# Optimization experiments

Hardware: AMD Instinct MI355X
Metric: run time of the kernel (lower is better)

## Reference

```python
import jax, jax.numpy as jnp
import numpy as np

B, S, H, D = 4, 2048, 16, 64
E = H * D  # embed_dim = 1024


def setup_inputs() -> dict:
    key = jax.random.key(0)
    kq, kk, kv, kw, kb = jax.random.split(key, 5)
    query = jax.random.normal(kq, (B, S, H, D), dtype=jnp.float32)
    key_t = jax.random.normal(kk, (B, S, H, D), dtype=jnp.float32)
    value = jax.random.normal(kv, (B, S, H, D), dtype=jnp.float32)
    qkv_proj = jnp.zeros((1,), dtype=jnp.float32)  # unused arg in original forward
    # causal mask (0 = masked), matching masked_fill(attn_mask == 0, -inf)
    attn_mask = jnp.tril(jnp.ones((S, S), dtype=jnp.int32))
    bound = 1.0 / np.sqrt(E)
    out_w = jax.random.uniform(kw, (E, E), jnp.float32, -bound, bound)
    out_b = jax.random.uniform(kb, (E,), jnp.float32, -bound, bound)
    return {"query": query, "key": key_t, "value": value, "qkv_proj": qkv_proj,
            "attn_mask": attn_mask, "out_w": out_w, "out_b": out_b}


def reference(query, key, value, qkv_proj, attn_mask, out_w, out_b):
    # flatten heads: module does single-head attention over embed_dim
    q = query.reshape(B, S, E) * (float(E) ** -0.5)  # scaling uses embed_dim, per source
    k = key.reshape(B, S, E)
    v = value.reshape(B, S, E)
    scores = jnp.einsum('bqe,bke->bqk', q, k)  # [B,S,S]
    scores = jnp.where(attn_mask[None, :, :] == 0, -jnp.inf, scores)
    # safe softmax: subtract max, exp, normalize
    probs = jax.nn.softmax(scores, axis=-1)
    attn_out = jnp.einsum('bqk,bke->bqe', probs, v)  # [B,S,E]
    return attn_out @ out_w.T + out_b
```

## Files before the change

### kernel.cpp

```cpp
#include <hip/hip_runtime.h>


typedef __attribute__((ext_vector_type(8))) short bf16x8;
typedef __attribute__((ext_vector_type(4))) float floatx4;

#define MFMA16(a, b, c) __builtin_amdgcn_mfma_f32_16x16x32_bf16((a), (b), (c), 0, 0, 0)

#define B_ 4
#define S_ 2048
#define E_ 1024

static __device__ __forceinline__ unsigned short f2bf(float f) {
  unsigned int u = __float_as_uint(f);
  u += 0x7FFFu + ((u >> 16) & 1u);
  return (unsigned short)(u >> 16);
}
static __device__ __forceinline__ float bf2f(unsigned short h) {
  return __uint_as_float(((unsigned int)h) << 16);
}

#define STAGE_TILE_64(dst, srcbase, LD, k0, w, l)                              \
  _Pragma("unroll")                                                            \
  for (int i_ = 0; i_ < 4; ++i_) {                                             \
    int c_ = i_ * 256 + (w) * 64 + (l);                                        \
    int row_ = c_ >> 3, cg_ = c_ & 7;                                          \
    int col_ = (cg_ ^ (row_ & 7)) * 8;                                         \
    __builtin_amdgcn_global_load_lds(                                          \
        (const __attribute__((address_space(1))) unsigned int*)((srcbase) +    \
            (size_t)row_ * (LD) + (k0) + col_),                                \
        (__attribute__((address_space(3))) unsigned int*)((dst) +              \
            (size_t)(i_ * 256 + (w) * 64) * 8),                                \
        16, 0, 0);                                                             \
  }

static __device__ __forceinline__ const bf16x8* frag_at(
    const unsigned short* base, int row, int cg) {
  return (const bf16x8*)(base + (size_t)row * 64 + ((cg ^ (row & 7)) * 8));
}

__global__ void cvt_all_kernel(const float* __restrict__ Q,
                               const float* __restrict__ K,
                               const float* __restrict__ W,
                               unsigned short* __restrict__ Qbf,
                               unsigned short* __restrict__ Kbf,
                               unsigned short* __restrict__ Wbf) {
  const int nQK = (B_ * S_ * E_) / 4;
  const int nW  = (E_ * E_) / 4;
  const int total = 2 * nQK + nW;
  int i = blockIdx.x * blockDim.x + threadIdx.x;
  int stride = gridDim.x * blockDim.x;
  for (; i < total; i += stride) {
    const float* src; unsigned short* dst; float sc; int j;
    if (i < nQK)            { src = Q; dst = Qbf; sc = 0.03125f; j = i; }
    else if (i < 2 * nQK)   { src = K; dst = Kbf; sc = 1.0f; j = i - nQK; }
    else                    { src = W; dst = Wbf; sc = 1.0f; j = i - 2 * nQK; }
    float4 v = ((const float4*)src)[j];
    ushort4 o;
    o.x = f2bf(v.x * sc); o.y = f2bf(v.y * sc);
    o.z = f2bf(v.z * sc); o.w = f2bf(v.w * sc);
    ((ushort4*)dst)[j] = o;
  }
}

__global__ void transpose_v_kernel(const float* __restrict__ V,
                                   unsigned short* __restrict__ Vt) {
  __shared__ float tile[32][33];
  int bid = blockIdx.x;
  int eb = (bid & 31) * 32;
  int sb = ((bid >> 5) & 63) * 32;
  int b  = bid >> 11;
  int tx = threadIdx.x & 31, ty = threadIdx.x >> 5;
  const float* src = V + ((size_t)(b * S_ + sb)) * E_ + eb;
#pragma unroll
  for (int i = 0; i < 4; ++i) {
    int sl = ty + i * 8;
    tile[sl][tx] = src[(size_t)sl * E_ + tx];
  }
  __syncthreads();
  unsigned short* dst = Vt + ((size_t)(b * E_ + eb)) * S_ + sb;
#pragma unroll
  for (int i = 0; i < 4; ++i) {
    int el = ty + i * 8;
    dst[(size_t)el * S_ + tx] = f2bf(tile[tx][el]);
  }
}

__global__ __launch_bounds__(256, 4) void qk_kernel(
    const unsigned short* __restrict__ A,
    const unsigned short* __restrict__ Bw,
    unsigned short* __restrict__ SP,
    float* __restrict__ rsp) {
  __shared__ unsigned short At[128 * 64];
  __shared__ unsigned short Bt[128 * 64];
  __shared__ float rs_l[2][128];
  const int bid0 = blockIdx.x;
  const int bid = (bid0 & 7) * 68 + (bid0 >> 3);
  const int b = bid / 136;
  const int ti = bid - b * 136;
  float fr = sqrtf(8.0f * (float)ti + 1.0f);
  int trow = (int)((fr - 1.0f) * 0.5f);
  if ((trow + 1) * (trow + 2) / 2 <= ti) ++trow;
  else if (trow * (trow + 1) / 2 > ti) --trow;
  const int tcol = ti - trow * (trow + 1) / 2;
  const int bm = trow * 128, bn = tcol * 128;

  const int tid = threadIdx.x;
  const int w = tid >> 6, l = tid & 63;
  const int l15 = l & 15, l4 = l >> 4;
  const int wr = w >> 1, wc = w & 1;
  const unsigned short* Ab = A + (size_t)b * S_ * E_ + (size_t)bm * E_;
  const unsigned short* Bb = Bw + (size_t)b * S_ * E_ + (size_t)bn * E_;

  floatx4 acc[4][4];
#pragma unroll
  for (int m = 0; m < 4; ++m)
#pragma unroll
    for (int n = 0; n < 4; ++n) acc[m][n] = (floatx4)0.0f;

  for (int k0 = 0; k0 < E_; k0 += 64) {
    STAGE_TILE_64(At, Ab, E_, k0, w, l)
    STAGE_TILE_64(Bt, Bb, E_, k0, w, l)
    __syncthreads();
#pragma unroll
    for (int h = 0; h < 2; ++h) {
      bf16x8 af[4], bfv[4];
#pragma unroll
      for (int mf = 0; mf < 4; ++mf)
        af[mf] = *frag_at(At, wr * 64 + mf * 16 + l15, h * 4 + l4);
#pragma unroll
      for (int nf = 0; nf < 4; ++nf)
        bfv[nf] = *frag_at(Bt, wc * 64 + nf * 16 + l15, h * 4 + l4);
#pragma unroll
      for (int mf = 0; mf < 4; ++mf)
#pragma unroll
        for (int nf = 0; nf < 4; ++nf)
          acc[mf][nf] = MFMA16(af[mf], bfv[nf], acc[mf][nf]);
    }
    __syncthreads();
  }

  float ps[16];
#pragma unroll
  for (int i = 0; i < 16; ++i) ps[i] = 0.0f;
  unsigned short* Cb = SP + (size_t)b * S_ * S_;
#pragma unroll
  for (int mf = 0; mf < 4; ++mf)
#pragma unroll
    for (int nf = 0; nf < 4; ++nf)
#pragma unroll
      for (int r = 0; r < 4; ++r) {
        int row = bm + wr * 64 + mf * 16 + l4 * 4 + r;
        int col = bn + wc * 64 + nf * 16 + l15;
        float p = (col <= row) ? __expf(acc[mf][nf][r]) : 0.0f;
        ps[mf * 4 + r] += p;
        Cb[(size_t)row * S_ + col] = f2bf(p);
      }
#pragma unroll
  for (int i = 0; i < 16; ++i) {
    float s = ps[i];
    s += __shfl_xor(s, 1);
    s += __shfl_xor(s, 2);
    s += __shfl_xor(s, 4);
    s += __shfl_xor(s, 8);
    ps[i] = s;
  }
  if (l15 == 0) {
#pragma unroll
    for (int mf = 0; mf < 4; ++mf)
#pragma unroll
      for (int r = 0; r < 4; ++r)
        rs_l[wc][wr * 64 + mf * 16 + l4 * 4 + r] = ps[mf * 4 + r];
  }
  __syncthreads();
  if (tid < 128)
    rsp[((size_t)(b * S_ + bm + tid)) * 17 + tcol] = rs_l[0][tid] + rs_l[1][tid];
}

__global__ __launch_bounds__(256) void reduce_rsp_kernel(
    const float* __restrict__ rsp, float* __restrict__ rsum) {
  int row = blockIdx.x * 256 + threadIdx.x;
  const int ntile = ((row & 2047) >> 7) + 1;
  const float* rp = rsp + (size_t)row * 17;
  float s = 0.0f;
  for (int t = 0; t < ntile; ++t) s += rp[t];
  rsum[row] = s;
}

__global__ __launch_bounds__(256, 3) void pv_kernel(
    const unsigned short* __restrict__ P,
    const unsigned short* __restrict__ Vt,
    const float* __restrict__ rsumG,
    unsigned short* __restrict__ Abf) {
  __shared__ unsigned short At[128 * 64];
  __shared__ unsigned short Bt[128 * 64];
  const int bid0 = blockIdx.x;
  const int x = bid0 & 7;
  const int j = bid0 >> 3;
  const int b = x >> 1;
  const int nt = (x & 1) * 4 + (j & 3);
  const int r2 = j >> 2;
  const int mt = (r2 < 8) ? r2 : 23 - r2;
  const int bm = mt * 128, bn = nt * 128;

  const int tid = threadIdx.x;
  const int w = tid >> 6, l = tid & 63;
  const int l15 = l & 15, l4 = l >> 4;
  const int wr = w >> 1, wc = w & 1;
  const unsigned short* Ab = P + (size_t)b * S_ * S_ + (size_t)bm * S_;
  const unsigned short* Bb = Vt + (size_t)b * E_ * S_ + (size_t)bn * S_;

  floatx4 acc[4][4];
#pragma unroll
  for (int m = 0; m < 4; ++m)
#pragma unroll
    for (int n = 0; n < 4; ++n) acc[m][n] = (floatx4)0.0f;

  const int kmax = (mt + 1) * 128;
  for (int k0 = 0; k0 < kmax; k0 += 64) {
    STAGE_TILE_64(At, Ab, S_, k0, w, l)
    STAGE_TILE_64(Bt, Bb, S_, k0, w, l)
    __syncthreads();
#pragma unroll
    for (int h = 0; h < 2; ++h) {
      bf16x8 af[4], bfv[4];
#pragma unroll
      for (int mf = 0; mf < 4; ++mf)
        af[mf] = *frag_at(At, wr * 64 + mf * 16 + l15, h * 4 + l4);
#pragma unroll
      for (int nf = 0; nf < 4; ++nf)
        bfv[nf] = *frag_at(Bt, wc * 64 + nf * 16 + l15, h * 4 + l4);
#pragma unroll
      for (int mf = 0; mf < 4; ++mf)
#pragma unroll
        for (int nf = 0; nf < 4; ++nf)
          acc[mf][nf] = MFMA16(af[mf], bfv[nf], acc[mf][nf]);
    }
    __syncthreads();
  }

  unsigned short* Cb = Abf + (size_t)b * S_ * E_;
  const float* rs = rsumG + (size_t)b * S_ + bm;
#pragma unroll
  for (int mf = 0; mf < 4; ++mf) {
    float inv[4];
#pragma unroll
    for (int r = 0; r < 4; ++r)
      inv[r] = 1.0f / rs[wr * 64 + mf * 16 + l4 * 4 + r];
#pragma unroll
    for (int nf = 0; nf < 4; ++nf)
#pragma unroll
      for (int r = 0; r < 4; ++r) {
        int row = bm + wr * 64 + mf * 16 + l4 * 4 + r;
        int col = bn + wc * 64 + nf * 16 + l15;
        Cb[(size_t)row * E_ + col] = f2bf(acc[mf][nf][r] * inv[r]);
      }
  }
}

__global__ __launch_bounds__(256, 3) void proj_kernel(
    const unsigned short* __restrict__ A,
    const unsigned short* __restrict__ Bw,
    const float* __restrict__ bias,
    float* __restrict__ C) {
  __shared__ unsigned short At[128 * 64];
  __shared__ unsigned short Bt[128 * 64];
  const int bid0 = blockIdx.x;
  const int bid = (bid0 & 7) * 64 + (bid0 >> 3);
  const int tid = threadIdx.x;
  const int w = tid >> 6, l = tid & 63;
  const int l15 = l & 15, l4 = l >> 4;
  const int wr = w >> 1, wc = w & 1;
  const int bm = (bid >> 3) * 128;
  const int bn = (bid & 7) * 128;
  const unsigned short* Ab = A + (size_t)bm * E_;
  const unsigned short* Bb = Bw + (size_t)bn * E_;

  floatx4 acc[4][4];
#pragma unroll
  for (int m = 0; m < 4; ++m)
#pragma unroll
    for (int n = 0; n < 4; ++n) acc[m][n] = (floatx4)0.0f;

  for (int k0 = 0; k0 < E_; k0 += 64) {
    STAGE_TILE_64(At, Ab, E_, k0, w, l)
    STAGE_TILE_64(Bt, Bb, E_, k0, w, l)
    __syncthreads();
#pragma unroll
    for (int h = 0; h < 2; ++h) {
      bf16x8 af[4], bfv[4];
#pragma unroll
      for (int mf = 0; mf < 4; ++mf)
        af[mf] = *frag_at(At, wr * 64 + mf * 16 + l15, h * 4 + l4);
#pragma unroll
      for (int nf = 0; nf < 4; ++nf)
        bfv[nf] = *frag_at(Bt, wc * 64 + nf * 16 + l15, h * 4 + l4);
#pragma unroll
      for (int mf = 0; mf < 4; ++mf)
#pragma unroll
        for (int nf = 0; nf < 4; ++nf)
          acc[mf][nf] = MFMA16(af[mf], bfv[nf], acc[mf][nf]);
    }
    __syncthreads();
  }

  float bv[4];
#pragma unroll
  for (int nf = 0; nf < 4; ++nf) bv[nf] = bias[bn + wc * 64 + nf * 16 + l15];
#pragma unroll
  for (int mf = 0; mf < 4; ++mf)
#pragma unroll
    for (int nf = 0; nf < 4; ++nf)
#pragma unroll
      for (int r = 0; r < 4; ++r) {
        int row = bm + wr * 64 + mf * 16 + l4 * 4 + r;
        int col = bn + wc * 64 + nf * 16 + l15;
        C[(size_t)row * E_ + col] = acc[mf][nf][r] + bv[nf];
      }
}

extern "C" void kernel_launch(void* const* d_in, const int* in_sizes, int n_in,
                              void* d_out, int out_size, void* d_ws, size_t ws_size,
                              hipStream_t stream) {
  const float* Q    = (const float*)d_in[0];
  const float* Kf   = (const float*)d_in[1];
  const float* V    = (const float*)d_in[2];
  const float* W    = (const float*)d_in[5];
  const float* bias = (const float*)d_in[6];
  float* out = (float*)d_out;
  (void)ws_size;

  char* ws = (char*)d_ws;
  unsigned short* Qbf = (unsigned short*)(ws);
  unsigned short* Kbf = (unsigned short*)(ws + (size_t)(16u << 20));
  unsigned short* Vt  = (unsigned short*)(ws + (size_t)(32u << 20));
  unsigned short* Wbf = (unsigned short*)(ws + (size_t)(48u << 20));
  unsigned short* SP  = (unsigned short*)(ws + (size_t)(50u << 20));
  float*          rsp  = (float*)(ws + (size_t)(82u << 20));
  float*          rsum = (float*)(ws + (size_t)(83u << 20));
  unsigned short* Abf = Kbf;

  cvt_all_kernel<<<4096, 256, 0, stream>>>(Q, Kf, W, Qbf, Kbf, Wbf);
  transpose_v_kernel<<<B_ * (S_ / 32) * (E_ / 32), 256, 0, stream>>>(V, Vt);

  qk_kernel<<<B_ * 136, 256, 0, stream>>>(Qbf, Kbf, SP, rsp);
  reduce_rsp_kernel<<<(B_ * S_) / 256, 256, 0, stream>>>(rsp, rsum);
  pv_kernel<<<B_ * 16 * 8, 256, 0, stream>>>(SP, Vt, rsum, Abf);
  proj_kernel<<<(B_ * S_ / 128) * (E_ / 128), 256, 0, stream>>>(Abf, Wbf, bias, out);
}
```

Before: 114.4 us.

## Reassociate output projection into V before the PV GEMM and drop the transpose

The attention is computed as P·(V·Wᵀ) instead of (P·V)·Wᵀ. A new GEMM computes U = W·Vᵀ per batch, stored transposed, and the PV kernel is replaced by a P·U kernel that applies the 1/rowsum normalisation and the bias and writes the fp32 output directly. V is now converted to bf16 inside the shared conversion kernel, so the separate transpose kernel goes away. The standalone projection kernel and the bf16 attention intermediate are removed too. FLOPs stay about the same, and the change adds a bf16 rounding of V·Wᵀ in place of the rounding of the attention output.

```diff
diff --git a/kernel.cpp b/kernel.cpp
--- a/kernel.cpp
+++ b/kernel.cpp
@@ -40,48 +40,28 @@
 
 __global__ void cvt_all_kernel(const float* __restrict__ Q,
                                const float* __restrict__ K,
+                               const float* __restrict__ V,
                                const float* __restrict__ W,
                                unsigned short* __restrict__ Qbf,
                                unsigned short* __restrict__ Kbf,
+                               unsigned short* __restrict__ Vbf,
                                unsigned short* __restrict__ Wbf) {
   const int nQK = (B_ * S_ * E_) / 4;
   const int nW  = (E_ * E_) / 4;
-  const int total = 2 * nQK + nW;
+  const int total = 3 * nQK + nW;
   int i = blockIdx.x * blockDim.x + threadIdx.x;
   int stride = gridDim.x * blockDim.x;
   for (; i < total; i += stride) {
     const float* src; unsigned short* dst; float sc; int j;
     if (i < nQK)            { src = Q; dst = Qbf; sc = 0.03125f; j = i; }
     else if (i < 2 * nQK)   { src = K; dst = Kbf; sc = 1.0f; j = i - nQK; }
-    else                    { src = W; dst = Wbf; sc = 1.0f; j = i - 2 * nQK; }
+    else if (i < 3 * nQK)   { src = V; dst = Vbf; sc = 1.0f; j = i - 2 * nQK; }
+    else                    { src = W; dst = Wbf; sc = 1.0f; j = i - 3 * nQK; }
     float4 v = ((const float4*)src)[j];
     ushort4 o;
     o.x = f2bf(v.x * sc); o.y = f2bf(v.y * sc);
     o.z = f2bf(v.z * sc); o.w = f2bf(v.w * sc);
     ((ushort4*)dst)[j] = o;
-  }
-}
-
-__global__ void transpose_v_kernel(const float* __restrict__ V,
-                                   unsigned short* __restrict__ Vt) {
-  __shared__ float tile[32][33];
-  int bid = blockIdx.x;
-  int eb = (bid & 31) * 32;
-  int sb = ((bid >> 5) & 63) * 32;
-  int b  = bid >> 11;
-  int tx = threadIdx.x & 31, ty = threadIdx.x >> 5;
-  const float* src = V + ((size_t)(b * S_ + sb)) * E_ + eb;
-#pragma unroll
-  for (int i = 0; i < 4; ++i) {
-    int sl = ty + i * 8;
-    tile[sl][tx] = src[(size_t)sl * E_ + tx];
-  }
-  __syncthreads();
-  unsigned short* dst = Vt + ((size_t)(b * E_ + eb)) * S_ + sb;
-#pragma unroll
-  for (int i = 0; i < 4; ++i) {
-    int el = ty + i * 8;
-    dst[(size_t)el * S_ + tx] = f2bf(tile[tx][el]);
   }
 }
 
@@ -186,11 +166,73 @@
   rsum[row] = s;
 }
 
-__global__ __launch_bounds__(256, 3) void pv_kernel(
+__global__ __launch_bounds__(256, 3) void vw_kernel(
+    const unsigned short* __restrict__ Wbf,
+    const unsigned short* __restrict__ Vbf,
+    unsigned short* __restrict__ Ut) {
+  __shared__ unsigned short At[128 * 64];
+  __shared__ unsigned short Bt[128 * 64];
+  const int bid0 = blockIdx.x;
+  const int bid = (bid0 & 7) * 64 + (bid0 >> 3);
+  const int b = bid >> 7;
+  const int mt = (bid >> 4) & 7;
+  const int nt = bid & 15;
+  const int bm = mt * 128, bn = nt * 128;
+
+  const int tid = threadIdx.x;
+  const int w = tid >> 6, l = tid & 63;
+  const int l15 = l & 15, l4 = l >> 4;
+  const int wr = w >> 1, wc = w & 1;
+  const unsigned short* Ab = Wbf + (size_t)bm * E_;
+  const unsigned short* Bb = Vbf + (size_t)b * S_ * E_ + (size_t)bn * E_;
+
+  floatx4 acc[4][4];
+#pragma unroll
+  for (int m = 0; m < 4; ++m)
+#pragma unroll
+    for (int n = 0; n < 4; ++n) acc[m][n] = (floatx4)0.0f;
+
+  for (int k0 = 0; k0 < E_; k0 += 64) {
+    STAGE_TILE_64(At, Ab, E_, k0, w, l)
+    STAGE_TILE_64(Bt, Bb, E_, k0, w, l)
+    __syncthreads();
+#pragma unroll
+    for (int h = 0; h < 2; ++h) {
+      bf16x8 af[4], bfv[4];
+#pragma unroll
+      for (int mf = 0; mf < 4; ++mf)
+        af[mf] = *frag_at(At, wr * 64 + mf * 16 + l15, h * 4 + l4);
+#pragma unroll
+      for (int nf = 0; nf < 4; ++nf)
+        bfv[nf] = *frag_at(Bt, wc * 64 + nf * 16 + l15, h * 4 + l4);
+#pragma unroll
+      for (int mf = 0; mf < 4; ++mf)
+#pragma unroll
+        for (int nf = 0; nf < 4; ++nf)
+          acc[mf][nf] = MFMA16(af[mf], bfv[nf], acc[mf][nf]);
+    }
+    __syncthreads();
+  }
+
+  unsigned short* Cb = Ut + (size_t)b * E_ * S_;
+#pragma unroll
+  for (int mf = 0; mf < 4; ++mf)
+#pragma unroll
+    for (int nf = 0; nf < 4; ++nf)
+#pragma unroll
+      for (int r = 0; r < 4; ++r) {
+        int row = bm + wr * 64 + mf * 16 + l4 * 4 + r;
+        int col = bn + wc * 64 + nf * 16 + l15;
+        Cb[(size_t)row * S_ + col] = f2bf(acc[mf][nf][r]);
+      }
+}
+
+__global__ __launch_bounds__(256, 3) void pu_kernel(
     const unsigned short* __restrict__ P,
-    const unsigned short* __restrict__ Vt,
+    const unsigned short* __restrict__ Ut,
     const float* __restrict__ rsumG,
-    unsigned short* __restrict__ Abf) {
+    const float* __restrict__ bias,
+    float* __restrict__ out) {
   __shared__ unsigned short At[128 * 64];
   __shared__ unsigned short Bt[128 * 64];
   const int bid0 = blockIdx.x;
@@ -207,7 +249,7 @@
   const int l15 = l & 15, l4 = l >> 4;
   const int wr = w >> 1, wc = w & 1;
   const unsigned short* Ab = P + (size_t)b * S_ * S_ + (size_t)bm * S_;
-  const unsigned short* Bb = Vt + (size_t)b * E_ * S_ + (size_t)bn * S_;
+  const unsigned short* Bb = Ut + (size_t)b * E_ * S_ + (size_t)bn * S_;
 
   floatx4 acc[4][4];
 #pragma unroll
@@ -238,8 +280,11 @@
     __syncthreads();
   }
 
-  unsigned short* Cb = Abf + (size_t)b * S_ * E_;
+  float* Cb = out + (size_t)b * S_ * E_;
   const float* rs = rsumG + (size_t)b * S_ + bm;
+  float bv[4];
+#pragma unroll
+  for (int nf = 0; nf < 4; ++nf) bv[nf] = bias[bn + wc * 64 + nf * 16 + l15];
 #pragma unroll
   for (int mf = 0; mf < 4; ++mf) {
     float inv[4];
@@ -252,70 +297,9 @@
       for (int r = 0; r < 4; ++r) {
         int row = bm + wr * 64 + mf * 16 + l4 * 4 + r;
         int col = bn + wc * 64 + nf * 16 + l15;
-        Cb[(size_t)row * E_ + col] = f2bf(acc[mf][nf][r] * inv[r]);
+        Cb[(size_t)row * E_ + col] = acc[mf][nf][r] * inv[r] + bv[nf];
       }
   }
-}
-
-__global__ __launch_bounds__(256, 3) void proj_kernel(
-    const unsigned short* __restrict__ A,
-    const unsigned short* __restrict__ Bw,
-    const float* __restrict__ bias,
-    float* __restrict__ C) {
-  __shared__ unsigned short At[128 * 64];
-  __shared__ unsigned short Bt[128 * 64];
-  const int bid0 = blockIdx.x;
-  const int bid = (bid0 & 7) * 64 + (bid0 >> 3);
-  const int tid = threadIdx.x;
-  const int w = tid >> 6, l = tid & 63;
-  const int l15 = l & 15, l4 = l >> 4;
-  const int wr = w >> 1, wc = w & 1;
-  const int bm = (bid >> 3) * 128;
-  const int bn = (bid & 7) * 128;
-  const unsigned short* Ab = A + (size_t)bm * E_;
-  const unsigned short* Bb = Bw + (size_t)bn * E_;
-
-  floatx4 acc[4][4];
-#pragma unroll
-  for (int m = 0; m < 4; ++m)
-#pragma unroll
-    for (int n = 0; n < 4; ++n) acc[m][n] = (floatx4)0.0f;
-
-  for (int k0 = 0; k0 < E_; k0 += 64) {
-    STAGE_TILE_64(At, Ab, E_, k0, w, l)
-    STAGE_TILE_64(Bt, Bb, E_, k0, w, l)
-    __syncthreads();
-#pragma unroll
-    for (int h = 0; h < 2; ++h) {
-      bf16x8 af[4], bfv[4];
-#pragma unroll
-      for (int mf = 0; mf < 4; ++mf)
-        af[mf] = *frag_at(At, wr * 64 + mf * 16 + l15, h * 4 + l4);
-#pragma unroll
-      for (int nf = 0; nf < 4; ++nf)
-        bfv[nf] = *frag_at(Bt, wc * 64 + nf * 16 + l15, h * 4 + l4);
-#pragma unroll
-      for (int mf = 0; mf < 4; ++mf)
-#pragma unroll
-        for (int nf = 0; nf < 4; ++nf)
-          acc[mf][nf] = MFMA16(af[mf], bfv[nf], acc[mf][nf]);
-    }
-    __syncthreads();
-  }
-
-  float bv[4];
-#pragma unroll
-  for (int nf = 0; nf < 4; ++nf) bv[nf] = bias[bn + wc * 64 + nf * 16 + l15];
-#pragma unroll
-  for (int mf = 0; mf < 4; ++mf)
-#pragma unroll
-    for (int nf = 0; nf < 4; ++nf)
-#pragma unroll
-      for (int r = 0; r < 4; ++r) {
-        int row = bm + wr * 64 + mf * 16 + l4 * 4 + r;
-        int col = bn + wc * 64 + nf * 16 + l15;
-        C[(size_t)row * E_ + col] = acc[mf][nf][r] + bv[nf];
-      }
 }
 
 extern "C" void kernel_launch(void* const* d_in, const int* in_sizes, int n_in,
@@ -332,18 +316,17 @@
   char* ws = (char*)d_ws;
   unsigned short* Qbf = (unsigned short*)(ws);
   unsigned short* Kbf = (unsigned short*)(ws + (size_t)(16u << 20));
-  unsigned short* Vt  = (unsigned short*)(ws + (size_t)(32u << 20));
+  unsigned short* Vbf = (unsigned short*)(ws + (size_t)(32u << 20));
   unsigned short* Wbf = (unsigned short*)(ws + (size_t)(48u << 20));
   unsigned short* SP  = (unsigned short*)(ws + (size_t)(50u << 20));
   float*          rsp  = (float*)(ws + (size_t)(82u << 20));
   float*          rsum = (float*)(ws + (size_t)(83u << 20));
-  unsigned short* Abf = Kbf;
-
-  cvt_all_kernel<<<4096, 256, 0, stream>>>(Q, Kf, W, Qbf, Kbf, Wbf);
-  transpose_v_kernel<<<B_ * (S_ / 32) * (E_ / 32), 256, 0, stream>>>(V, Vt);
+  unsigned short* Ut = Qbf;
+
+  cvt_all_kernel<<<4096, 256, 0, stream>>>(Q, Kf, V, W, Qbf, Kbf, Vbf, Wbf);
 
   qk_kernel<<<B_ * 136, 256, 0, stream>>>(Qbf, Kbf, SP, rsp);
   reduce_rsp_kernel<<<(B_ * S_) / 256, 256, 0, stream>>>(rsp, rsum);
-  pv_kernel<<<B_ * 16 * 8, 256, 0, stream>>>(SP, Vt, rsum, Abf);
-  proj_kernel<<<(B_ * S_ / 128) * (E_ / 128), 256, 0, stream>>>(Abf, Wbf, bias, out);
-}
+  vw_kernel<<<512, 256, 0, stream>>>(Wbf, Vbf, Ut);
+  pu_kernel<<<512, 256, 0, stream>>>(SP, Ut, rsum, bias, out);
+}
```

Result: no change. 112.6 us (-1.6%).
